# Kernel optimization log

Measured on AMD Instinct MI355X. Metric: run time of the kernel, lower is better.

## Reference

```python
import jax, jax.numpy as jnp
import numpy as np

B, T, D, H, S, PM = 2048, 128, 32, 256, 39, 12


def setup_inputs() -> dict:
    key = jax.random.key(0)
    ks = jax.random.split(key, 20)
    s = 0.05
    return {
        "x": jax.random.normal(ks[0], (B, T, D), jnp.float32),
        "latlons": jax.random.normal(ks[1], (B, 2), jnp.float32),
        "yearly_aggs": jax.random.normal(ks[2], (B, 37), jnp.float32),
        "pred_month": jax.random.uniform(ks[3], (B, PM), jnp.float32),
        # EA-LSTM cell parameters (Linear stores weight as [out,in])
        "Wf_i": jax.random.normal(ks[4], (H, D), jnp.float32) * s,
        "Wf_h": jax.random.normal(ks[5], (H, H), jnp.float32) * s,
        "bf_h": jnp.zeros((H,), jnp.float32),
        "Wu": jax.random.normal(ks[6], (H, S), jnp.float32) * s,
        "bu": jnp.zeros((H,), jnp.float32),
        "Wg_i": jax.random.normal(ks[7], (H, D), jnp.float32) * s,
        "Wg_h": jax.random.normal(ks[8], (H, H), jnp.float32) * s,
        "bg_h": jnp.zeros((H,), jnp.float32),
        "Wo_i": jax.random.normal(ks[9], (H, D), jnp.float32) * s,
        "Wo_h": jax.random.normal(ks[10], (H, H), jnp.float32) * s,
        "bo_h": jnp.zeros((H,), jnp.float32),
        # dense head: [268 -> 256 -> 1], no nonlinearity between layers (as in source)
        "Wd0": jax.random.normal(ks[11], (256, H + PM), jnp.float32) * s,
        "bd0": jnp.zeros((256,), jnp.float32),
        "Wd1": jax.random.normal(ks[12], (1, 256), jnp.float32) * s,
        "bd1": jnp.zeros((1,), jnp.float32),
    }


def reference(x, latlons, yearly_aggs, pred_month,
              Wf_i, Wf_h, bf_h, Wu, bu,
              Wg_i, Wg_h, bg_h, Wo_i, Wo_h, bo_h,
              Wd0, bd0, Wd1, bd1):
    x_s = jnp.concatenate([latlons, yearly_aggs], axis=-1)  # [B,S]
    i_gate = jax.nn.sigmoid(x_s @ Wu.T + bu)  # [B,H], static input gate

    # Precompute the input-to-gate projections for all timesteps (one big GEMM each)
    pf = jnp.einsum('btd,hd->tbh', x, Wf_i)  # [T,B,H]
    pg = jnp.einsum('btd,hd->tbh', x, Wg_i)
    po = jnp.einsum('btd,hd->tbh', x, Wo_i)

    h0 = jnp.zeros((x.shape[0], Wf_h.shape[0]), x.dtype)
    c0 = jnp.zeros_like(h0)

    def step(carry, inp):
        h, c = carry
        pf_t, pg_t, po_t = inp
        f = jax.nn.sigmoid(pf_t + h @ Wf_h.T + bf_h)
        g = jnp.tanh(pg_t + h @ Wg_h.T + bg_h)
        o = jax.nn.sigmoid(po_t + h @ Wo_h.T + bo_h)
        c1 = f * c + i_gate * g
        h1 = o * jnp.tanh(c1)
        return (h1, c1), None

    (h_last, _), _ = jax.lax.scan(step, (h0, c0), (pf, pg, po))

    # only the last hidden state feeds the dense head (dropout p=0 -> identity)
    z = jnp.concatenate([h_last, pred_month], axis=-1)  # [B, H+12]
    z = z @ Wd0.T + bd0
    z = z @ Wd1.T + bd1
    return z  # [B,1]
```

## Files before the change

### kernel.cpp

```cpp
#include <hip/hip_runtime.h>

typedef __bf16 bf16x8 __attribute__((ext_vector_type(8)));
typedef float  f32x4  __attribute__((ext_vector_type(4)));
typedef int    v4i    __attribute__((ext_vector_type(4)));

#define LOG2E 1.4426950408889634f

__device__ __forceinline__ float fexp(float x){ return __builtin_amdgcn_exp2f(x * LOG2E); }
__device__ __forceinline__ float sigm(float x){ return __builtin_amdgcn_rcpf(1.0f + fexp(-x)); }
__device__ __forceinline__ float ftanh(float x){
  float r = __builtin_amdgcn_rcpf(1.0f + __builtin_amdgcn_exp2f(-2.0f*LOG2E*x));
  return 2.0f*r - 1.0f;
}
__device__ __forceinline__ f32x4 MFMA(bf16x8 a, bf16x8 b, f32x4 c){
  return __builtin_amdgcn_mfma_f32_16x16x32_bf16(a, b, c, 0, 0, 0);
}
#define BC(w) __builtin_bit_cast(v4i, (w))

#define GRP_A(LEAD, A_, KT_) asm volatile(LEAD                  \
    "v_mfma_f32_16x16x32_bf16 %0, %6, %7, %0\n\t"               \
    "v_mfma_f32_16x16x32_bf16 %1, %6, %8, %1\n\t"               \
    "v_mfma_f32_16x16x32_bf16 %2, %6, %9, %2\n\t"               \
    "v_mfma_f32_16x16x32_bf16 %3, %6, %10, %3\n\t"              \
    "v_mfma_f32_16x16x32_bf16 %4, %6, %11, %4\n\t"              \
    "v_mfma_f32_16x16x32_bf16 %5, %6, %12, %5\n\t"              \
    "s_nop 3"                                                   \
    : "+v"(acc0),"+v"(acc1),"+v"(acc2),"+v"(acc3),"+v"(acc4),"+v"(acc5) \
    : "v"(A_), "a"(awf[(KT_)]),"a"(awf[(KT_)+5]),"a"(awf[(KT_)+10]),    \
      "a"(awf[(KT_)+15]),"a"(awf[(KT_)+20]),"a"(awf[(KT_)+25]))

#define GRP_V(A_, O_) asm volatile(                             \
    "v_mfma_f32_16x16x32_bf16 %0, %6, %7, %0\n\t"               \
    "v_mfma_f32_16x16x32_bf16 %1, %6, %8, %1\n\t"               \
    "v_mfma_f32_16x16x32_bf16 %2, %6, %9, %2\n\t"               \
    "v_mfma_f32_16x16x32_bf16 %3, %6, %10, %3\n\t"              \
    "v_mfma_f32_16x16x32_bf16 %4, %6, %11, %4\n\t"              \
    "v_mfma_f32_16x16x32_bf16 %5, %6, %12, %5\n\t"              \
    "s_nop 3"                                                   \
    : "+v"(acc0),"+v"(acc1),"+v"(acc2),"+v"(acc3),"+v"(acc4),"+v"(acc5) \
    : "v"(A_), "v"(wvf[(O_)]),"v"(wvf[(O_)+2]),"v"(wvf[(O_)+4]),        \
      "v"(wvf[(O_)+6]),"v"(wvf[(O_)+8]),"v"(wvf[(O_)+10]))

#define GRP_LX(A7_, AX_) asm volatile(                          \
    "ds_read_b128 %6, %14\n\t"                                  \
    "ds_read_b128 %7, %14 offset:1024\n\t"                      \
    "ds_read_b128 %8, %14 offset:16384\n\t"                     \
    "ds_read_b128 %9, %14 offset:17408\n\t"                     \
    "ds_read_b128 %10, %14 offset:32768\n\t"                    \
    "ds_read_b128 %11, %14 offset:33792\n\t"                    \
    "s_waitcnt lgkmcnt(0)\n\t"                                  \
    "v_mfma_f32_16x16x32_bf16 %0, %12, %6, %0\n\t"              \
    "v_mfma_f32_16x16x32_bf16 %1, %12, %7, %1\n\t"              \
    "v_mfma_f32_16x16x32_bf16 %2, %12, %8, %2\n\t"              \
    "v_mfma_f32_16x16x32_bf16 %3, %12, %9, %3\n\t"              \
    "v_mfma_f32_16x16x32_bf16 %4, %12, %10, %4\n\t"             \
    "v_mfma_f32_16x16x32_bf16 %5, %12, %11, %5\n\t"             \
    "ds_read_b128 %6, %15\n\t"                                  \
    "ds_read_b128 %7, %15 offset:1024\n\t"                      \
    "ds_read_b128 %8, %15 offset:16384\n\t"                     \
    "ds_read_b128 %9, %15 offset:17408\n\t"                     \
    "ds_read_b128 %10, %15 offset:32768\n\t"                    \
    "ds_read_b128 %11, %15 offset:33792\n\t"                    \
    "s_waitcnt lgkmcnt(0)\n\t"                                  \
    "v_mfma_f32_16x16x32_bf16 %0, %13, %6, %0\n\t"              \
    "v_mfma_f32_16x16x32_bf16 %1, %13, %7, %1\n\t"              \
    "v_mfma_f32_16x16x32_bf16 %2, %13, %8, %2\n\t"              \
    "v_mfma_f32_16x16x32_bf16 %3, %13, %9, %3\n\t"              \
    "v_mfma_f32_16x16x32_bf16 %4, %13, %10, %4\n\t"             \
    "v_mfma_f32_16x16x32_bf16 %5, %13, %11, %5\n\t"             \
    "s_nop 3"                                                   \
    : "+v"(acc0),"+v"(acc1),"+v"(acc2),"+v"(acc3),"+v"(acc4),"+v"(acc5), \
      "=&v"(t0),"=&v"(t1),"=&v"(t2),"=&v"(t3),"=&v"(t4),"=&v"(t5)        \
    : "v"(A7_), "v"(AX_), "v"(waddr0), "v"(waddr1))

#define BARRIER() asm volatile("s_waitcnt lgkmcnt(0)\n\ts_barrier" ::: "memory")

__global__ void
__attribute__((amdgpu_flat_work_group_size(512,512), amdgpu_waves_per_eu(2,2)))
ealstm_kernel(
    const float* __restrict__ x,      const float* __restrict__ latlons,
    const float* __restrict__ yearly, const float* __restrict__ pm,
    const float* __restrict__ Wf_i, const float* __restrict__ Wf_h, const float* __restrict__ bf_h,
    const float* __restrict__ Wu,   const float* __restrict__ bu,
    const float* __restrict__ Wg_i, const float* __restrict__ Wg_h, const float* __restrict__ bg_h,
    const float* __restrict__ Wo_i, const float* __restrict__ Wo_h, const float* __restrict__ bo_h,
    const float* __restrict__ Wd0,  const float* __restrict__ bd0,
    const float* __restrict__ Wd1,  const float* __restrict__ bd1,
    float* __restrict__ out)
{
  __shared__ __align__(16) __bf16 hbuf[2][4096];
  __shared__ __align__(16) __bf16 xbuf[2][16*40];
  __shared__ __align__(16) __bf16 wlds[2*48*512];
  __shared__ __align__(16) float  xs[16*64];

  const int tid  = threadIdx.x;
  const int w    = tid >> 6;
  const int lane = tid & 63;
  const int q    = lane >> 4;
  const int l    = lane & 15;
  const int wgb  = blockIdx.x * 8;

  const float* Wh[3] = {Wf_h, Wg_h, Wo_h};
  const float* Wi[3] = {Wf_i, Wg_i, Wo_i};

  for(int idx = tid; idx < 16*64; idx += 512){
    int m = idx >> 6, k = idx & 63;
    float v = 0.0f;
    if(m < 8){
      int b = wgb + m;
      if(k < 2) v = latlons[b*2 + k];
      else if(k < 39) v = yearly[b*37 + (k-2)];
    }
    xs[idx] = v;
  }
  for(int idx = tid; idx < 2*4096; idx += 512) ((__bf16*)hbuf)[idx] = (__bf16)0.0f;
  {
    int buf = tid >> 8, r = 8 + ((tid >> 5) & 7), c = tid & 31;
    xbuf[buf][r*40 + c] = (__bf16)0.0f;
  }
  if(tid < 256){
    int m = tid >> 5, k = tid & 31;
    xbuf[0][m*40 + k] = (__bf16)x[(size_t)(wgb + m)*4096 + k];
  }
  for(int grp = tid; grp < 2*48*64; grp += 512){
    int frag = grp >> 6, ln = grp & 63;
    int kk = frag / 48, f2 = frag % 48;
    int g = f2 >> 4, nt = f2 & 15;
    int q2 = ln >> 4, l2 = ln & 15;
    int cc = nt*16 + l2;
    const float* p = (kk == 0) ? (Wh[g] + cc*256 + 224 + q2*8)
                               : (Wi[g] + cc*32  + q2*8);
    bf16x8 v;
    #pragma unroll
    for(int j=0;j<8;j++) v[j] = (__bf16)p[j];
    *(bf16x8*)&wlds[frag*512 + ln*8] = v;
  }

  const int  srcl = lane & 31;
  const bool lo   = lane < 32;
  const int  qq4  = (q & 1) * 4;
  const int  colw = w*32 + ((lane & 32) >> 1) + l;
  const int  hwb  = (colw >> 5)*512 + qq4*32 + ((colw >> 3) & 3)*8 + (colw & 7);
  const unsigned waddr0 = (unsigned)(unsigned long long)&wlds[(0*48 + w*2)*512 + lane*8];
  const unsigned waddr1 = waddr0 + 49152u;
  const float b3f = bf_h[colw], b3g = bg_h[colw], b3o = bo_h[colw];

  __syncthreads();

  f32x4 igv;
  {
    float bu0 = bu[w*32 + l], bu1 = bu[w*32 + 16 + l];
    f32x4 iga0 = {bu0,bu0,bu0,bu0};
    f32x4 iga1 = {bu1,bu1,bu1,bu1};
    #pragma unroll
    for(int kt=0; kt<2; kt++){
      bf16x8 a;
      const float* xr = &xs[l*64 + kt*32 + q*8];
      #pragma unroll
      for(int j=0;j<8;j++) a[j] = (__bf16)xr[j];
      #pragma unroll
      for(int n=0;n<2;n++){
        int cc = w*32 + n*16 + l;
        bf16x8 b;
        #pragma unroll
        for(int j=0;j<8;j++){
          int k = kt*32 + q*8 + j;
          b[j] = (__bf16)((k < 39) ? Wu[cc*39 + k] : 0.0f);
        }
        if(n == 0) iga0 = MFMA(a, b, iga0); else iga1 = MFMA(a, b, iga1);
      }
    }
    #pragma unroll
    for(int i=0;i<4;i++){
      float s0 = sigm(iga0[i]);
      float s1 = __shfl(sigm(iga1[i]), srcl);
      igv[i] = lo ? s0 : s1;
    }
  }

  v4i wvf[12];
  #pragma unroll
  for(int f = 0; f < 12; f++){
    int gn = f >> 1, kt = 5 + (f & 1);
    int g = gn >> 1, n = gn & 1;
    int cc = w*32 + n*16 + l;
    const float* p = Wh[g] + cc*256 + kt*32 + q*8;
    f32x4 v0 = *(const f32x4*)p;
    f32x4 v1 = *(const f32x4*)(p + 4);
    bf16x8 v;
    v[0]=(__bf16)v0[0]; v[1]=(__bf16)v0[1]; v[2]=(__bf16)v0[2]; v[3]=(__bf16)v0[3];
    v[4]=(__bf16)v1[0]; v[5]=(__bf16)v1[1]; v[6]=(__bf16)v1[2]; v[7]=(__bf16)v1[3];
    wvf[f] = BC(v);
    if((f & 3) == 3) asm volatile("" ::: "memory");
  }
  v4i awf[30];
  #pragma unroll
  for(int f = 0; f < 30; f++){
    int gn = f / 5, kt = f % 5;
    int g = gn >> 1, n = gn & 1;
    int cc = w*32 + n*16 + l;
    const float* p = Wh[g] + cc*256 + kt*32 + q*8;
    f32x4 v0 = *(const f32x4*)p;
    f32x4 v1 = *(const f32x4*)(p + 4);
    bf16x8 v;
    v[0]=(__bf16)v0[0]; v[1]=(__bf16)v0[1]; v[2]=(__bf16)v0[2]; v[3]=(__bf16)v0[3];
    v[4]=(__bf16)v1[0]; v[5]=(__bf16)v1[1]; v[6]=(__bf16)v1[2]; v[7]=(__bf16)v1[3];
    asm("" : "=a"(awf[f]) : "0"(BC(v)));
    if((f % 5) == 4) asm volatile("" ::: "memory");
  }

  f32x4 cst = {0.f, 0.f, 0.f, 0.f};

  const int xri = (lane >> 2)*40 + (lane & 3)*8;
  const float* xbase = x + (size_t)(wgb + (lane >> 2))*4096 + (lane & 3)*8;
  f32x4 pv0 = {0.f,0.f,0.f,0.f}, pv1 = {0.f,0.f,0.f,0.f};
  if(w == 7 && lane < 32){
    pv0 = *(const f32x4*)(xbase + 32);
    pv1 = *(const f32x4*)(xbase + 36);
  }
  asm volatile("" ::: "memory");

#define LSTM_STEP(T_, CUR_)                                                     \
  {                                                                             \
      \
      \
    if(w == 7 && lane < 32){                                                    \
      if((T_) < 127){                                                           \
        bf16x8 v;                                                               \
        v[0]=(__bf16)pv0[0]; v[1]=(__bf16)pv0[1]; v[2]=(__bf16)pv0[2]; v[3]=(__bf16)pv0[3]; \
        v[4]=(__bf16)pv1[0]; v[5]=(__bf16)pv1[1]; v[6]=(__bf16)pv1[2]; v[7]=(__bf16)pv1[3]; \
        *(bf16x8*)&xbuf[(CUR_) ^ 1][xri] = v;                                   \
      }                                                                         \
      if((T_) < 126){                                                           \
        pv0 = *(const f32x4*)(xbase + ((T_)+2)*32);                             \
        pv1 = *(const f32x4*)(xbase + ((T_)+2)*32 + 4);                         \
      }                                                                         \
    }                                                                           \
    asm volatile("" ::: "memory");                                              \
    f32x4 z4 = {0.f,0.f,0.f,0.f};                                               \
    v4i acc0 = BC(z4), acc1 = BC(z4), acc2 = BC(z4);                            \
    v4i acc3 = BC(z4), acc4 = BC(z4), acc5 = BC(z4);                            \
    v4i t0, t1, t2, t3, t4, t5;                                                 \
    const __bf16* hb = hbuf[CUR_];                                              \
    { v4i a = BC(*(const bf16x8*)&hb[0*512 + l*32 + q*8]); GRP_A("s_nop 3\n\t", a, 0); } \
    { v4i a = BC(*(const bf16x8*)&hb[1*512 + l*32 + q*8]); GRP_A("", a, 1); }   \
    { v4i a = BC(*(const bf16x8*)&hb[2*512 + l*32 + q*8]); GRP_A("", a, 2); }   \
    { v4i a = BC(*(const bf16x8*)&hb[3*512 + l*32 + q*8]); GRP_A("", a, 3); }   \
    { v4i a = BC(*(const bf16x8*)&hb[4*512 + l*32 + q*8]); GRP_A("", a, 4); }   \
    { v4i a = BC(*(const bf16x8*)&hb[5*512 + l*32 + q*8]); GRP_V(a, 0); }       \
    { v4i a = BC(*(const bf16x8*)&hb[6*512 + l*32 + q*8]); GRP_V(a, 1); }       \
    { v4i a7 = BC(*(const bf16x8*)&hb[7*512 + l*32 + q*8]);                     \
      v4i ax = BC(*(const bf16x8*)&xbuf[CUR_][l*40 + q*8]);                     \
      GRP_LX(a7, ax); }                                                         \
    asm volatile("s_nop 7\n\ts_nop 7\n\ts_nop 7"                                \
      : "+v"(acc0),"+v"(acc1),"+v"(acc2),"+v"(acc3),"+v"(acc4),"+v"(acc5));     \
    f32x4 a0 = __builtin_bit_cast(f32x4, acc0);                                 \
    f32x4 a1 = __builtin_bit_cast(f32x4, acc1);                                 \
    f32x4 a2 = __builtin_bit_cast(f32x4, acc2);                                 \
    f32x4 a3 = __builtin_bit_cast(f32x4, acc3);                                 \
    f32x4 a4 = __builtin_bit_cast(f32x4, acc4);                                 \
    f32x4 a5 = __builtin_bit_cast(f32x4, acc5);                                 \
    _Pragma("unroll")                                                           \
    for(int i=0;i<4;i++){                                                       \
      float f1 = __shfl(a1[i], srcl);                                           \
      float g1 = __shfl(a3[i], srcl);                                           \
      float o1 = __shfl(a5[i], srcl);                                           \
      float fv = sigm ((lo ? a0[i] : f1) + b3f);                                \
      float gv = ftanh((lo ? a2[i] : g1) + b3g);                                \
      float ov = sigm ((lo ? a4[i] : o1) + b3o);                                \
      float cc = fv * cst[i] + igv[i] * gv;                                     \
      cst[i] = cc;                                                              \
      hbuf[(CUR_) ^ 1][hwb + i*32] = (__bf16)(ov * ftanh(cc));                  \
    }                                                                           \
    BARRIER();                                                                  \
  }

  #pragma unroll 1
  for(int tt = 0; tt < 64; tt++){
    LSTM_STEP(2*tt,     0)
    LSTM_STEP(2*tt + 1, 1)
  }
#undef LSTM_STEP

  f32x4 hd[2];
  { f32x4 z4 = {0.f,0.f,0.f,0.f}; hd[0] = z4; hd[1] = z4; }
  #pragma unroll 2
  for(int kt=0; kt<8; kt++){
    bf16x8 a = *(const bf16x8*)&hbuf[0][kt*512 + l*32 + q*8];
    #pragma unroll
    for(int n=0;n<2;n++){
      int cc = w*32 + n*16 + l;
      const float* p = Wd0 + cc*268 + kt*32 + q*8;
      bf16x8 b;
      #pragma unroll
      for(int j=0;j<8;j++) b[j] = (__bf16)p[j];
      hd[n] = MFMA(a, b, hd[n]);
    }
  }
  {
    bf16x8 a;
    #pragma unroll
    for(int j=0;j<8;j++){
      int k2 = q*8 + j;
      a[j] = (__bf16)((l < 8 && k2 < 12) ? pm[(size_t)(wgb + l)*12 + k2] : 0.0f);
    }
    #pragma unroll
    for(int n=0;n<2;n++){
      int cc = w*32 + n*16 + l;
      bf16x8 b;
      #pragma unroll
      for(int j=0;j<8;j++){
        int k2 = q*8 + j;
        b[j] = (__bf16)((k2 < 12) ? Wd0[cc*268 + 256 + k2] : 0.0f);
      }
      hd[n] = MFMA(a, b, hd[n]);
    }
  }
  float* z1 = (float*)wlds;
  #pragma unroll
  for(int n=0;n<2;n++){
    int cc = w*32 + n*16 + l;
    float bb = bd0[cc];
    #pragma unroll
    for(int i=0;i<4;i++) z1[(q*4 + i)*264 + cc] = hd[n][i] + bb;
  }
  __syncthreads();
  if(tid < 256){
    int row = tid >> 5, seg = tid & 31;
    const float* zr = &z1[row*264 + seg*8];
    const float* wr = Wd1 + seg*8;
    float s = 0.0f;
    #pragma unroll
    for(int j=0;j<8;j++) s += zr[j] * wr[j];
    s += __shfl_xor(s, 1);
    s += __shfl_xor(s, 2);
    s += __shfl_xor(s, 4);
    s += __shfl_xor(s, 8);
    s += __shfl_xor(s, 16);
    if(seg == 0) out[wgb + row] = s + bd1[0];
  }
}

extern "C" void kernel_launch(void* const* d_in, const int* in_sizes, int n_in,
                              void* d_out, int out_size, void* d_ws, size_t ws_size,
                              hipStream_t stream) {
  const float* x       = (const float*)d_in[0];
  const float* latlons = (const float*)d_in[1];
  const float* yearly  = (const float*)d_in[2];
  const float* pm      = (const float*)d_in[3];
  const float* Wf_i    = (const float*)d_in[4];
  const float* Wf_h    = (const float*)d_in[5];
  const float* bf_h    = (const float*)d_in[6];
  const float* Wu      = (const float*)d_in[7];
  const float* bu      = (const float*)d_in[8];
  const float* Wg_i    = (const float*)d_in[9];
  const float* Wg_h    = (const float*)d_in[10];
  const float* bg_h    = (const float*)d_in[11];
  const float* Wo_i    = (const float*)d_in[12];
  const float* Wo_h    = (const float*)d_in[13];
  const float* bo_h    = (const float*)d_in[14];
  const float* Wd0     = (const float*)d_in[15];
  const float* bd0     = (const float*)d_in[16];
  const float* Wd1     = (const float*)d_in[17];
  const float* bd1     = (const float*)d_in[18];

  ealstm_kernel<<<dim3(256), dim3(512), 0, stream>>>(
      x, latlons, yearly, pm,
      Wf_i, Wf_h, bf_h, Wu, bu,
      Wg_i, Wg_h, bg_h, Wo_i, Wo_h, bo_h,
      Wd0, bd0, Wd1, bd1,
      (float*)d_out);
}
```

Baseline: 354.0 us.

## Swizzle h buffer in LDS, prefetch LDS weight tiles earlier, use AGPR accumulators

Applies an XOR swizzle to the hidden-state LDS layout so that row reads for the MFMA A operand and scattered h writes avoid bank conflicts. It also splits the tail weight-read group so the first batch of LDS weight reads is issued before the VGPR-weight MFMA groups, hiding LDS latency behind compute. Two of the six accumulators are moved to AGPRs to relieve VGPR pressure. The risks are extra index arithmetic on the write path and possible register-move overhead when AGPR accumulators are read back for the activation math.

```diff
diff --git a/kernel.cpp b/kernel.cpp
--- a/kernel.cpp
+++ b/kernel.cpp
@@ -25,7 +25,7 @@
     "v_mfma_f32_16x16x32_bf16 %4, %6, %11, %4\n\t"              \
     "v_mfma_f32_16x16x32_bf16 %5, %6, %12, %5\n\t"              \
     "s_nop 3"                                                   \
-    : "+v"(acc0),"+v"(acc1),"+v"(acc2),"+v"(acc3),"+v"(acc4),"+v"(acc5) \
+    : "+v"(acc0),"+v"(acc1),"+v"(acc2),"+v"(acc3),"+a"(acc4),"+a"(acc5) \
     : "v"(A_), "a"(awf[(KT_)]),"a"(awf[(KT_)+5]),"a"(awf[(KT_)+10]),    \
       "a"(awf[(KT_)+15]),"a"(awf[(KT_)+20]),"a"(awf[(KT_)+25]))
 
@@ -37,17 +37,21 @@
     "v_mfma_f32_16x16x32_bf16 %4, %6, %11, %4\n\t"              \
     "v_mfma_f32_16x16x32_bf16 %5, %6, %12, %5\n\t"              \
     "s_nop 3"                                                   \
-    : "+v"(acc0),"+v"(acc1),"+v"(acc2),"+v"(acc3),"+v"(acc4),"+v"(acc5) \
+    : "+v"(acc0),"+v"(acc1),"+v"(acc2),"+v"(acc3),"+a"(acc4),"+a"(acc5) \
     : "v"(A_), "v"(wvf[(O_)]),"v"(wvf[(O_)+2]),"v"(wvf[(O_)+4]),        \
       "v"(wvf[(O_)+6]),"v"(wvf[(O_)+8]),"v"(wvf[(O_)+10]))
 
-#define GRP_LX(A7_, AX_) asm volatile(                          \
-    "ds_read_b128 %6, %14\n\t"                                  \
-    "ds_read_b128 %7, %14 offset:1024\n\t"                      \
-    "ds_read_b128 %8, %14 offset:16384\n\t"                     \
-    "ds_read_b128 %9, %14 offset:17408\n\t"                     \
-    "ds_read_b128 %10, %14 offset:32768\n\t"                    \
-    "ds_read_b128 %11, %14 offset:33792\n\t"                    \
+#define GRP_R(ADDR_) asm volatile(                              \
+    "ds_read_b128 %0, %6\n\t"                                   \
+    "ds_read_b128 %1, %6 offset:1024\n\t"                       \
+    "ds_read_b128 %2, %6 offset:16384\n\t"                      \
+    "ds_read_b128 %3, %6 offset:17408\n\t"                      \
+    "ds_read_b128 %4, %6 offset:32768\n\t"                      \
+    "ds_read_b128 %5, %6 offset:33792"                          \
+    : "=&v"(t0),"=&v"(t1),"=&v"(t2),"=&v"(t3),"=&v"(t4),"=&v"(t5)       \
+    : "v"(ADDR_))
+
+#define GRP_X0(A7_) asm volatile(                               \
     "s_waitcnt lgkmcnt(0)\n\t"                                  \
     "v_mfma_f32_16x16x32_bf16 %0, %12, %6, %0\n\t"              \
     "v_mfma_f32_16x16x32_bf16 %1, %12, %7, %1\n\t"              \
@@ -55,23 +59,27 @@
     "v_mfma_f32_16x16x32_bf16 %3, %12, %9, %3\n\t"              \
     "v_mfma_f32_16x16x32_bf16 %4, %12, %10, %4\n\t"             \
     "v_mfma_f32_16x16x32_bf16 %5, %12, %11, %5\n\t"             \
-    "ds_read_b128 %6, %15\n\t"                                  \
-    "ds_read_b128 %7, %15 offset:1024\n\t"                      \
-    "ds_read_b128 %8, %15 offset:16384\n\t"                     \
-    "ds_read_b128 %9, %15 offset:17408\n\t"                     \
-    "ds_read_b128 %10, %15 offset:32768\n\t"                    \
-    "ds_read_b128 %11, %15 offset:33792\n\t"                    \
+    "ds_read_b128 %6, %13\n\t"                                  \
+    "ds_read_b128 %7, %13 offset:1024\n\t"                      \
+    "ds_read_b128 %8, %13 offset:16384\n\t"                     \
+    "ds_read_b128 %9, %13 offset:17408\n\t"                     \
+    "ds_read_b128 %10, %13 offset:32768\n\t"                    \
+    "ds_read_b128 %11, %13 offset:33792"                        \
+    : "+v"(acc0),"+v"(acc1),"+v"(acc2),"+v"(acc3),"+a"(acc4),"+a"(acc5), \
+      "+v"(t0),"+v"(t1),"+v"(t2),"+v"(t3),"+v"(t4),"+v"(t5)              \
+    : "v"(A7_), "v"(waddr1))
+
+#define GRP_X1(AX_) asm volatile(                               \
     "s_waitcnt lgkmcnt(0)\n\t"                                  \
-    "v_mfma_f32_16x16x32_bf16 %0, %13, %6, %0\n\t"              \
-    "v_mfma_f32_16x16x32_bf16 %1, %13, %7, %1\n\t"              \
-    "v_mfma_f32_16x16x32_bf16 %2, %13, %8, %2\n\t"              \
-    "v_mfma_f32_16x16x32_bf16 %3, %13, %9, %3\n\t"              \
-    "v_mfma_f32_16x16x32_bf16 %4, %13, %10, %4\n\t"             \
-    "v_mfma_f32_16x16x32_bf16 %5, %13, %11, %5\n\t"             \
+    "v_mfma_f32_16x16x32_bf16 %0, %12, %6, %0\n\t"              \
+    "v_mfma_f32_16x16x32_bf16 %1, %12, %7, %1\n\t"              \
+    "v_mfma_f32_16x16x32_bf16 %2, %12, %8, %2\n\t"              \
+    "v_mfma_f32_16x16x32_bf16 %3, %12, %9, %3\n\t"              \
+    "v_mfma_f32_16x16x32_bf16 %4, %12, %10, %4\n\t"             \
+    "v_mfma_f32_16x16x32_bf16 %5, %12, %11, %5\n\t"             \
     "s_nop 3"                                                   \
-    : "+v"(acc0),"+v"(acc1),"+v"(acc2),"+v"(acc3),"+v"(acc4),"+v"(acc5), \
-      "=&v"(t0),"=&v"(t1),"=&v"(t2),"=&v"(t3),"=&v"(t4),"=&v"(t5)        \
-    : "v"(A7_), "v"(AX_), "v"(waddr0), "v"(waddr1))
+    : "+v"(acc0),"+v"(acc1),"+v"(acc2),"+v"(acc3),"+a"(acc4),"+a"(acc5) \
+    : "v"(t0),"v"(t1),"v"(t2),"v"(t3),"v"(t4),"v"(t5), "v"(AX_))
 
 #define BARRIER() asm volatile("s_waitcnt lgkmcnt(0)\n\ts_barrier" ::: "memory")
 
@@ -140,7 +148,10 @@
   const bool lo   = lane < 32;
   const int  qq4  = (q & 1) * 4;
   const int  colw = w*32 + ((lane & 32) >> 1) + l;
-  const int  hwb  = (colw >> 5)*512 + qq4*32 + ((colw >> 3) & 3)*8 + (colw & 7);
+  const int  sl   = (l + (l >> 2)) & 3;
+  const int  aRowBase = l*32 + ((q ^ sl) << 3);
+  const int  hwbase = (colw >> 5)*512 + (colw & 7);
+  const int  chn    = (colw >> 3) & 3;
   const unsigned waddr0 = (unsigned)(unsigned long long)&wlds[(0*48 + w*2)*512 + lane*8];
   const unsigned waddr1 = waddr0 + 49152u;
   const float b3f = bf_h[colw], b3g = bg_h[colw], b3o = bo_h[colw];
@@ -222,8 +233,6 @@
 
 #define LSTM_STEP(T_, CUR_)                                                     \
   {                                                                             \
-      \
-      \
     if(w == 7 && lane < 32){                                                    \
       if((T_) < 127){                                                           \
         bf16x8 v;                                                               \
@@ -242,18 +251,18 @@
     v4i acc3 = BC(z4), acc4 = BC(z4), acc5 = BC(z4);                            \
     v4i t0, t1, t2, t3, t4, t5;                                                 \
     const __bf16* hb = hbuf[CUR_];                                              \
-    { v4i a = BC(*(const bf16x8*)&hb[0*512 + l*32 + q*8]); GRP_A("s_nop 3\n\t", a, 0); } \
-    { v4i a = BC(*(const bf16x8*)&hb[1*512 + l*32 + q*8]); GRP_A("", a, 1); }   \
-    { v4i a = BC(*(const bf16x8*)&hb[2*512 + l*32 + q*8]); GRP_A("", a, 2); }   \
-    { v4i a = BC(*(const bf16x8*)&hb[3*512 + l*32 + q*8]); GRP_A("", a, 3); }   \
-    { v4i a = BC(*(const bf16x8*)&hb[4*512 + l*32 + q*8]); GRP_A("", a, 4); }   \
-    { v4i a = BC(*(const bf16x8*)&hb[5*512 + l*32 + q*8]); GRP_V(a, 0); }       \
-    { v4i a = BC(*(const bf16x8*)&hb[6*512 + l*32 + q*8]); GRP_V(a, 1); }       \
-    { v4i a7 = BC(*(const bf16x8*)&hb[7*512 + l*32 + q*8]);                     \
-      v4i ax = BC(*(const bf16x8*)&xbuf[CUR_][l*40 + q*8]);                     \
-      GRP_LX(a7, ax); }                                                         \
+    { v4i a = BC(*(const bf16x8*)&hb[0*512 + aRowBase]); GRP_A("s_nop 3\n\t", a, 0); } \
+    { v4i a = BC(*(const bf16x8*)&hb[1*512 + aRowBase]); GRP_A("", a, 1); }     \
+    { v4i a = BC(*(const bf16x8*)&hb[2*512 + aRowBase]); GRP_A("", a, 2); }     \
+    { v4i a = BC(*(const bf16x8*)&hb[3*512 + aRowBase]); GRP_A("", a, 3); }     \
+    { v4i a = BC(*(const bf16x8*)&hb[4*512 + aRowBase]); GRP_A("", a, 4); }     \
+    GRP_R(waddr0);                                                              \
+    { v4i a = BC(*(const bf16x8*)&hb[5*512 + aRowBase]); GRP_V(a, 0); }         \
+    { v4i a = BC(*(const bf16x8*)&hb[6*512 + aRowBase]); GRP_V(a, 1); }         \
+    { v4i a7 = BC(*(const bf16x8*)&hb[7*512 + aRowBase]); GRP_X0(a7); }         \
+    { v4i ax = BC(*(const bf16x8*)&xbuf[CUR_][l*40 + q*8]); GRP_X1(ax); }       \
     asm volatile("s_nop 7\n\ts_nop 7\n\ts_nop 7"                                \
-      : "+v"(acc0),"+v"(acc1),"+v"(acc2),"+v"(acc3),"+v"(acc4),"+v"(acc5));     \
+      : "+v"(acc0),"+v"(acc1),"+v"(acc2),"+v"(acc3),"+a"(acc4),"+a"(acc5));     \
     f32x4 a0 = __builtin_bit_cast(f32x4, acc0);                                 \
     f32x4 a1 = __builtin_bit_cast(f32x4, acc1);                                 \
     f32x4 a2 = __builtin_bit_cast(f32x4, acc2);                                 \
@@ -270,7 +279,9 @@
       float ov = sigm ((lo ? a4[i] : o1) + b3o);                                \
       float cc = fv * cst[i] + igv[i] * gv;                                     \
       cst[i] = cc;                                                              \
-      hbuf[(CUR_) ^ 1][hwb + i*32] = (__bf16)(ov * ftanh(cc));                  \
+      int r = qq4 + i;                                                          \
+      int sr = (r + (r >> 2)) & 3;                                              \
+      hbuf[(CUR_) ^ 1][hwbase + r*32 + ((chn ^ sr) << 3)] = (__bf16)(ov * ftanh(cc)); \
     }                                                                           \
     BARRIER();                                                                  \
   }
@@ -286,7 +297,7 @@
   { f32x4 z4 = {0.f,0.f,0.f,0.f}; hd[0] = z4; hd[1] = z4; }
   #pragma unroll 2
   for(int kt=0; kt<8; kt++){
-    bf16x8 a = *(const bf16x8*)&hbuf[0][kt*512 + l*32 + q*8];
+    bf16x8 a = *(const bf16x8*)&hbuf[0][kt*512 + aRowBase];
     #pragma unroll
     for(int n=0;n<2;n++){
       int cc = w*32 + n*16 + l;
```

Result: slower. 440.8 us (+24.5%).
